# Kernel optimization log

Hardware: AMD Instinct MI355X
Metric: run time of the kernel (lower is better)

The kernel has to match this reference:

```python
import jax, jax.numpy as jnp
import numpy as np

N, E = 50000, 600000
IN_DIM, HID, OUT = 512, 256, 64
NEG_SLOPE = 0.2  # pyg GATConv default negative_slope


def setup_inputs() -> dict:
    key = jax.random.key(0)
    ks = jax.random.split(key, 6)
    features = jax.random.normal(ks[0], (N, IN_DIM), jnp.float32)
    edge_index = jax.random.randint(ks[1], (2, E), 0, N)
    W1 = jax.random.normal(ks[2], (IN_DIM, HID), jnp.float32) * (1.0 / np.sqrt(IN_DIM))
    W2 = jax.random.normal(ks[3], (HID, OUT), jnp.float32) * (1.0 / np.sqrt(HID))
    att_src = jax.random.normal(ks[4], (HID,), jnp.float32) * 0.1
    att_dst = jax.random.normal(ks[5], (HID,), jnp.float32) * 0.1
    return {"features": features, "W1": W1, "W2": W2,
            "att_src": att_src, "att_dst": att_dst, "edge_index": edge_index}


def _gat_propagate(h_pre, a_src, a_dst, src, dst, n):
    """STAGATE GATConv message passing (heads=1, concat=False, no self loops).

    Per-edge logit = leaky_relu(alpha_src[src] + alpha_dst[dst]),
    softmax over edges sharing the same dst, scatter-add of weighted src feats.
    """
    logits = jax.nn.leaky_relu(a_src[src] + a_dst[dst], NEG_SLOPE)        # [E]
    m = jax.ops.segment_max(logits, dst, num_segments=n)                   # [N]
    ex = jnp.exp(logits - m[dst])                                          # [E]
    denom = jax.ops.segment_sum(ex, dst, num_segments=n)                   # [N]
    w = ex / (denom[dst] + 1e-16)                                          # [E], pyg softmax eps
    return jax.ops.segment_sum(h_pre[src] * w[:, None], dst, num_segments=n)  # [N, C]


def reference(features, W1, W2, att_src, att_dst, edge_index):
    src, dst = edge_index[0], edge_index[1]
    n = features.shape[0]
    # conv1: attention computed and cached (self.attentions)
    hp1 = features @ W1                      # [N, HID]
    a_s = hp1 @ att_src                      # [N] per-node src attention score
    a_d = hp1 @ att_dst                      # [N] per-node dst attention score
    h1 = jax.nn.elu(_gat_propagate(hp1, a_s, a_d, src, dst, n))
    # conv2: attention=False -> plain linear
    h2 = h1 @ W2                             # [N, OUT]
    # conv3: weights = conv2.lin_src.T, tied_attention = conv1.attentions
    hp3 = h2 @ W2.T                          # [N, HID]
    h3 = jax.nn.elu(_gat_propagate(hp3, a_s, a_d, src, dst, n))
    # conv4: weights = conv1.lin_src.T, attention=False
    h4 = h3 @ W1.T                           # [N, IN_DIM]
    return (h2, h4)
```

## Files before the change

### kernel.cpp

```cpp
#include <hip/hip_runtime.h>
#include <hip/hip_bf16.h>
#include <cstdint>
#include <cstddef>

#define IN_DIM 512
#define HID 256
#define OUTD 64
#define NEG_SLOPE 0.2f

typedef __attribute__((ext_vector_type(8))) __bf16 bfrag_t;
typedef __attribute__((ext_vector_type(4))) float facc_t;
typedef __attribute__((ext_vector_type(4))) unsigned int u32x4;

__device__ __forceinline__ float bf2f(unsigned short u) {
  return __uint_as_float(((unsigned int)u) << 16);
}
__device__ __forceinline__ unsigned short f2bf(float f) {
  unsigned int x = __float_as_uint(f);
  x = (x + 0x7FFFu + ((x >> 16) & 1u)) >> 16;
  return (unsigned short)x;
}

#define GLOAD_LDS16(g, l)                                              \
  __builtin_amdgcn_global_load_lds(                                    \
      (const __attribute__((address_space(1))) void*)(g),              \
      (__attribute__((address_space(3))) void*)(l), 16, 0, 0)

template <int BM, int BN>
__global__ __launch_bounds__(256) void gemm_bt(const unsigned short* __restrict__ A,
                                               const unsigned short* __restrict__ B,
                                               void* __restrict__ Craw,
                                               unsigned short* __restrict__ Cb,
                                               int M, int N, int K, int c32, int act) {
  constexpr int FM = BM / 32, FN = BN / 32;
  constexpr int RT = BM + BN;
  __shared__ __align__(16) unsigned short lds[RT * 32];

  const int bm0 = blockIdx.x * BM;
  const int bn0 = blockIdx.y * BN;
  const int tid = threadIdx.x;
  const int lane = tid & 63;
  const int wave = tid >> 6;
  const int wrow = (wave >> 1) * (BM / 2);
  const int wcol = (wave & 1) * (BN / 2);
  const int lr = lane & 15;
  const int quad = lane >> 4;
  const int swz = (quad ^ (lr & 3)) << 3;

  facc_t acc[FM][FN];
#pragma unroll
  for (int i = 0; i < FM; ++i)
#pragma unroll
    for (int j = 0; j < FN; ++j) acc[i][j] = (facc_t){0.f, 0.f, 0.f, 0.f};

  for (int k0 = 0; k0 < K; k0 += 32) {
    __syncthreads();
#pragma unroll
    for (int t = wave; t < RT / 16; t += 4) {
      const int r0 = t * 16;
      const int row = r0 + (lane >> 2);
      const int seg = (lane & 3) ^ (row & 3);
      const unsigned short* g;
      if (r0 < BM) {
        int gm = bm0 + row;
        if (gm >= M) gm = M - 1;
        g = A + (size_t)gm * K + k0 + seg * 8;
      } else {
        g = B + (size_t)(bn0 + row - BM) * K + k0 + seg * 8;
      }
      GLOAD_LDS16(g, lds + t * 512);
    }
    __syncthreads();

    bfrag_t a[FM], b[FN];
#pragma unroll
    for (int i = 0; i < FM; ++i)
      a[i] = *(const bfrag_t*)&lds[(wrow + i * 16 + lr) * 32 + swz];
#pragma unroll
    for (int j = 0; j < FN; ++j)
      b[j] = *(const bfrag_t*)&lds[(BM + wcol + j * 16 + lr) * 32 + swz];
#pragma unroll
    for (int i = 0; i < FM; ++i)
#pragma unroll
      for (int j = 0; j < FN; ++j)
        acc[i][j] = __builtin_amdgcn_mfma_f32_16x16x32_bf16(a[i], b[j], acc[i][j], 0, 0, 0);
  }

#pragma unroll
  for (int i = 0; i < FM; ++i)
#pragma unroll
    for (int r = 0; r < 4; ++r) {
      const int grow = bm0 + wrow + i * 16 + quad * 4 + r;
      if (grow < M) {
#pragma unroll
        for (int j = 0; j < FN; ++j) {
          const int gcol = bn0 + wcol + j * 16 + lr;
          float v = acc[i][j][r];
          if (act) v = v > 0.f ? v : (expf(v) - 1.f);
          if (c32) ((float*)Craw)[(size_t)grow * N + gcol] = v;
          else ((unsigned short*)Craw)[(size_t)grow * N + gcol] = f2bf(v);
          if (Cb) Cb[(size_t)grow * N + gcol] = f2bf(v);
        }
      }
    }
}

__global__ void cvt_feat(const float* __restrict__ in, unsigned short* __restrict__ out,
                         int n8) {
  const int i = blockIdx.x * 256 + threadIdx.x;
  if (i >= n8) return;
  const float4 f0 = ((const float4*)in)[i * 2];
  const float4 f1 = ((const float4*)in)[i * 2 + 1];
  u32x4 pk;
  pk.x = (unsigned int)f2bf(f0.x) | ((unsigned int)f2bf(f0.y) << 16);
  pk.y = (unsigned int)f2bf(f0.z) | ((unsigned int)f2bf(f0.w) << 16);
  pk.z = (unsigned int)f2bf(f1.x) | ((unsigned int)f2bf(f1.y) << 16);
  pk.w = (unsigned int)f2bf(f1.z) | ((unsigned int)f2bf(f1.w) << 16);
  ((u32x4*)out)[i] = pk;
}

__global__ void cvt_weights(const float* __restrict__ W1, const float* __restrict__ W2,
                            unsigned short* __restrict__ W1T, unsigned short* __restrict__ W1b,
                            unsigned short* __restrict__ W2T, unsigned short* __restrict__ W2b) {
  const int idx = blockIdx.x * 256 + threadIdx.x;
  if (idx < IN_DIM * HID) {
    const unsigned short b = f2bf(W1[idx]);
    W1b[idx] = b;
    const int r = idx >> 8, c = idx & 255;
    W1T[(size_t)c * IN_DIM + r] = b;
  }
  if (idx < HID * OUTD) {
    const unsigned short b = f2bf(W2[idx]);
    W2b[idx] = b;
    const int r = idx >> 6, c = idx & 63;
    W2T[(size_t)c * HID + r] = b;
  }
}

__global__ __launch_bounds__(256) void rowdot(const unsigned short* __restrict__ hp,
                                              const float* __restrict__ att_s,
                                              const float* __restrict__ att_d,
                                              float* __restrict__ as_, float* __restrict__ ad_,
                                              int n) {
  const int node = blockIdx.x * 4 + (threadIdx.x >> 6);
  if (node >= n) return;
  const int lane = threadIdx.x & 63;
  const unsigned short* row = hp + (size_t)node * HID + (lane << 2);
  float s = 0.f, d = 0.f;
#pragma unroll
  for (int j = 0; j < 4; ++j) {
    const float h = bf2f(row[j]);
    s += h * att_s[(lane << 2) + j];
    d += h * att_d[(lane << 2) + j];
  }
  for (int off = 32; off > 0; off >>= 1) {
    s += __shfl_down(s, off);
    d += __shfl_down(d, off);
  }
  if (lane == 0) { as_[node] = s; ad_[node] = d; }
}

__global__ void init_nodes(float* __restrict__ denom, int* __restrict__ deg, int n) {
  const int i = blockIdx.x * 256 + threadIdx.x;
  if (i < n) {
    denom[i] = 0.f;
    deg[i] = 0;
  }
}

__global__ void edge_pass1(const int* __restrict__ src, const int* __restrict__ dst,
                           const float* __restrict__ as_, const float* __restrict__ ad_,
                           float* __restrict__ eexp, float* __restrict__ denom,
                           int* __restrict__ deg, int E, int n) {
  const int e = blockIdx.x * 256 + threadIdx.x;
  if (e >= E) return;
  const int s = src[e], d = dst[e];
  if ((unsigned)s >= (unsigned)n || (unsigned)d >= (unsigned)n) return;
  float l = as_[s] + ad_[d];
  l = l > 0.f ? l : NEG_SLOPE * l;
  const float ex = expf(fminf(l, 60.f));
  eexp[e] = ex;
  atomicAdd(&denom[d], ex);
  atomicAdd(&deg[d], 1);
}

__global__ __launch_bounds__(256) void scan_reduce(const int* __restrict__ deg,
                                                   int* __restrict__ bsum, int n) {
  __shared__ int ws4[4];
  const int tid = threadIdx.x, lane = tid & 63, wid = tid >> 6;
  const int base = blockIdx.x * 2048 + tid * 8;
  int s = 0;
#pragma unroll
  for (int j = 0; j < 8; ++j) {
    const int i = base + j;
    if (i < n) s += deg[i];
  }
  for (int off = 32; off > 0; off >>= 1) s += __shfl_down(s, off);
  if (lane == 0) ws4[wid] = s;
  __syncthreads();
  if (tid == 0) bsum[blockIdx.x] = ws4[0] + ws4[1] + ws4[2] + ws4[3];
}

__global__ __launch_bounds__(256) void scan_final(const int* __restrict__ deg,
                                                  const int* __restrict__ bsum,
                                                  int* __restrict__ row_ptr,
                                                  int* __restrict__ cursor, int n) {
  __shared__ int wsum[4];
  __shared__ int blockoff;
  const int tid = threadIdx.x, lane = tid & 63, wid = tid >> 6;
  if (wid == 0) {
    int v = (lane < blockIdx.x) ? bsum[lane] : 0;
    for (int off = 32; off > 0; off >>= 1) v += __shfl_down(v, off);
    if (lane == 0) blockoff = v;
  }
  const int base = blockIdx.x * 2048 + tid * 8;
  int v[8], s = 0;
#pragma unroll
  for (int j = 0; j < 8; ++j) {
    const int i = base + j;
    v[j] = (i < n) ? deg[i] : 0;
    s += v[j];
  }
  int ws = s;
  for (int off = 1; off < 64; off <<= 1) {
    const int t = __shfl_up(ws, off);
    if (lane >= off) ws += t;
  }
  if (lane == 63) wsum[wid] = ws;
  __syncthreads();
  int woff = 0;
  for (int w_ = 0; w_ < wid; ++w_) woff += wsum[w_];
  int run = blockoff + woff + (ws - s);
#pragma unroll
  for (int j = 0; j < 8; ++j) {
    const int i = base + j;
    if (i < n) {
      cursor[i] = run;
      row_ptr[i + 1] = run + v[j];
    }
    run += v[j];
  }
  if (blockIdx.x == 0 && tid == 0) row_ptr[0] = 0;
}

__global__ void edge_scatter(const int* __restrict__ src, const int* __restrict__ dst,
                             const float* __restrict__ eexp, const float* __restrict__ denom,
                             int* __restrict__ cursor, int* __restrict__ csr_src,
                             float* __restrict__ csr_w, int E, int n) {
  const int e = blockIdx.x * 256 + threadIdx.x;
  if (e >= E) return;
  const int s = src[e], d = dst[e];
  if ((unsigned)s >= (unsigned)n || (unsigned)d >= (unsigned)n) return;
  const float w = eexp[e] / (denom[d] + 1e-16f);
  const int pos = atomicAdd(&cursor[d], 1);
  csr_src[pos] = s;
  csr_w[pos] = w;
}

__global__ __launch_bounds__(256) void gat_prop256(const unsigned short* __restrict__ hpre,
                                                   const int* __restrict__ row_ptr,
                                                   const int* __restrict__ csr_src,
                                                   const float* __restrict__ csr_w,
                                                   unsigned short* __restrict__ out, int n) {
  const int node = blockIdx.x * 4 + (threadIdx.x >> 6);
  if (node >= n) return;
  const int lane = threadIdx.x & 63;
  const int half = lane >> 5;
  const int lh = lane & 31;
  const int beg = row_ptr[node], end = row_ptr[node + 1];
  const unsigned short* base = hpre + (lh << 3);
  float a[8] = {0.f, 0.f, 0.f, 0.f, 0.f, 0.f, 0.f, 0.f};
  int e = beg;
  for (; e + 8 <= end; e += 8) {
#pragma unroll
    for (int u = 0; u < 4; ++u) {
      const int e2 = e + 2 * u + half;
      const int s = csr_src[e2];
      const float w = csr_w[e2];
      const u32x4 v = *(const u32x4*)(base + (size_t)s * HID);
      a[0] += w * bf2f((unsigned short)(v.x & 0xffffu));
      a[1] += w * bf2f((unsigned short)(v.x >> 16));
      a[2] += w * bf2f((unsigned short)(v.y & 0xffffu));
      a[3] += w * bf2f((unsigned short)(v.y >> 16));
      a[4] += w * bf2f((unsigned short)(v.z & 0xffffu));
      a[5] += w * bf2f((unsigned short)(v.z >> 16));
      a[6] += w * bf2f((unsigned short)(v.w & 0xffffu));
      a[7] += w * bf2f((unsigned short)(v.w >> 16));
    }
  }
  for (; e < end; e += 2) {
    const int e2 = e + half;
    if (e2 < end) {
      const int s = csr_src[e2];
      const float w = csr_w[e2];
      const u32x4 v = *(const u32x4*)(base + (size_t)s * HID);
      a[0] += w * bf2f((unsigned short)(v.x & 0xffffu));
      a[1] += w * bf2f((unsigned short)(v.x >> 16));
      a[2] += w * bf2f((unsigned short)(v.y & 0xffffu));
      a[3] += w * bf2f((unsigned short)(v.y >> 16));
      a[4] += w * bf2f((unsigned short)(v.z & 0xffffu));
      a[5] += w * bf2f((unsigned short)(v.z >> 16));
      a[6] += w * bf2f((unsigned short)(v.w & 0xffffu));
      a[7] += w * bf2f((unsigned short)(v.w >> 16));
    }
  }
#pragma unroll
  for (int i = 0; i < 8; ++i) a[i] += __shfl_xor(a[i], 32);
  if (half == 0) {
#pragma unroll
    for (int i = 0; i < 8; ++i) a[i] = a[i] > 0.f ? a[i] : (expf(a[i]) - 1.f);
    u32x4 o;
    o.x = (unsigned int)f2bf(a[0]) | ((unsigned int)f2bf(a[1]) << 16);
    o.y = (unsigned int)f2bf(a[2]) | ((unsigned int)f2bf(a[3]) << 16);
    o.z = (unsigned int)f2bf(a[4]) | ((unsigned int)f2bf(a[5]) << 16);
    o.w = (unsigned int)f2bf(a[6]) | ((unsigned int)f2bf(a[7]) << 16);
    *(u32x4*)(out + (size_t)node * HID + (lh << 3)) = o;
  }
}

__global__ __launch_bounds__(256) void gat_prop64(const unsigned short* __restrict__ hpre,
                                                  const int* __restrict__ row_ptr,
                                                  const int* __restrict__ csr_src,
                                                  const float* __restrict__ csr_w,
                                                  unsigned short* __restrict__ out, int n) {
  const int node = blockIdx.x * 4 + (threadIdx.x >> 6);
  if (node >= n) return;
  const int lane = threadIdx.x & 63;
  const int quad = lane >> 4;
  const int lr = lane & 15;
  const int beg = row_ptr[node], end = row_ptr[node + 1];
  const unsigned short* base = hpre + (lr << 2);
  float a0 = 0.f, a1 = 0.f, a2 = 0.f, a3 = 0.f;
  int e = beg;
  for (; e + 8 <= end; e += 8) {
#pragma unroll
    for (int u = 0; u < 2; ++u) {
      const int e2 = e + 4 * u + quad;
      const int s = csr_src[e2];
      const float w = csr_w[e2];
      const uint2 v = *(const uint2*)(base + (size_t)s * OUTD);
      a0 += w * bf2f((unsigned short)(v.x & 0xffffu));
      a1 += w * bf2f((unsigned short)(v.x >> 16));
      a2 += w * bf2f((unsigned short)(v.y & 0xffffu));
      a3 += w * bf2f((unsigned short)(v.y >> 16));
    }
  }
  for (; e < end; e += 4) {
    const int e2 = e + quad;
    if (e2 < end) {
      const int s = csr_src[e2];
      const float w = csr_w[e2];
      const uint2 v = *(const uint2*)(base + (size_t)s * OUTD);
      a0 += w * bf2f((unsigned short)(v.x & 0xffffu));
      a1 += w * bf2f((unsigned short)(v.x >> 16));
      a2 += w * bf2f((unsigned short)(v.y & 0xffffu));
      a3 += w * bf2f((unsigned short)(v.y >> 16));
    }
  }
  a0 += __shfl_xor(a0, 16); a0 += __shfl_xor(a0, 32);
  a1 += __shfl_xor(a1, 16); a1 += __shfl_xor(a1, 32);
  a2 += __shfl_xor(a2, 16); a2 += __shfl_xor(a2, 32);
  a3 += __shfl_xor(a3, 16); a3 += __shfl_xor(a3, 32);
  if (quad == 0) {
    uint2 o;
    o.x = (unsigned int)f2bf(a0) | ((unsigned int)f2bf(a1) << 16);
    o.y = (unsigned int)f2bf(a2) | ((unsigned int)f2bf(a3) << 16);
    *(uint2*)(out + (size_t)node * OUTD + (lr << 2)) = o;
  }
}

extern "C" void kernel_launch(void* const* d_in, const int* in_sizes, int n_in,
                              void* d_out, int out_size, void* d_ws, size_t ws_size,
                              hipStream_t stream) {
  const float* feat = (const float*)d_in[0];
  const float* W1 = (const float*)d_in[1];
  const float* W2 = (const float*)d_in[2];
  const float* att_s = (const float*)d_in[3];
  const float* att_d = (const float*)d_in[4];
  const int* ei = (const int*)d_in[5];
  const int N = in_sizes[0] / IN_DIM;
  const int E = in_sizes[5] / 2;
  const int* src = ei;
  const int* dst = ei + E;
  float* outf = (float*)d_out;

  unsigned short* featb = (unsigned short*)(outf + (size_t)N * OUTD);
  unsigned short* hp1 = featb + (size_t)N * IN_DIM;
  unsigned short* g2 = hp1 + (size_t)N * HID;

  char* w = (char*)d_ws;
  size_t off = 0;
  auto alloc = [&](size_t bytes) -> void* {
    void* p = w + off;
    off += (bytes + 255) & ~(size_t)255;
    return p;
  };
  unsigned short* h1h3 = (unsigned short*)alloc((size_t)N * HID * 2);
  unsigned short* h2b = (unsigned short*)alloc((size_t)N * OUTD * 2);
  float* a_src_v = (float*)alloc((size_t)N * 4);
  float* a_dst_v = (float*)alloc((size_t)N * 4);
  float* eexp = (float*)alloc((size_t)E * 4);
  float* denom = (float*)alloc((size_t)N * 4);
  int* deg = (int*)alloc((size_t)N * 4);
  int* row_ptr = (int*)alloc((size_t)(N + 1) * 4);
  int* cursor = (int*)alloc((size_t)N * 4);
  int* bsum = (int*)alloc((size_t)64 * 4);
  int* csr_src = (int*)alloc((size_t)E * 4);
  float* csr_w = (float*)alloc((size_t)E * 4);
  unsigned short* W1T = (unsigned short*)alloc((size_t)IN_DIM * HID * 2);
  unsigned short* W1b = (unsigned short*)alloc((size_t)IN_DIM * HID * 2);
  unsigned short* W2T = (unsigned short*)alloc((size_t)HID * OUTD * 2);
  unsigned short* W2b = (unsigned short*)alloc((size_t)HID * OUTD * 2);

  const int EB = (E + 255) / 256;
  const int NB = (N + 255) / 256;
  const int MB = (N + 127) / 128;
  const int SB = (N + 2047) / 2048;

  cvt_feat<<<(N * IN_DIM / 8 + 255) / 256, 256, 0, stream>>>(feat, featb, N * IN_DIM / 8);
  cvt_weights<<<(IN_DIM * HID + 255) / 256, 256, 0, stream>>>(W1, W2, W1T, W1b, W2T, W2b);

  gemm_bt<128, 128><<<dim3(MB, HID / 128), 256, 0, stream>>>(featb, W1T, hp1, nullptr,
                                                             N, HID, IN_DIM, 0, 0);
  rowdot<<<(N + 3) / 4, 256, 0, stream>>>(hp1, att_s, att_d, a_src_v, a_dst_v, N);

  init_nodes<<<NB, 256, 0, stream>>>(denom, deg, N);
  edge_pass1<<<EB, 256, 0, stream>>>(src, dst, a_src_v, a_dst_v, eexp, denom, deg, E, N);
  scan_reduce<<<SB, 256, 0, stream>>>(deg, bsum, N);
  scan_final<<<SB, 256, 0, stream>>>(deg, bsum, row_ptr, cursor, N);
  edge_scatter<<<EB, 256, 0, stream>>>(src, dst, eexp, denom, cursor, csr_src, csr_w, E, N);

  gat_prop256<<<(N + 3) / 4, 256, 0, stream>>>(hp1, row_ptr, csr_src, csr_w, h1h3, N);
  gemm_bt<128, 64><<<dim3(MB, OUTD / 64), 256, 0, stream>>>(h1h3, W2T, outf, h2b,
                                                            N, OUTD, HID, 1, 0);
  gat_prop64<<<(N + 3) / 4, 256, 0, stream>>>(h2b, row_ptr, csr_src, csr_w, g2, N);
  gemm_bt<128, 128><<<dim3(MB, HID / 128), 256, 0, stream>>>(g2, W2b, h1h3, nullptr,
                                                             N, HID, OUTD, 0, 1);
  gemm_bt<128, 128><<<dim3(MB, IN_DIM / 128), 256, 0, stream>>>(h1h3, W1b,
                                                                outf + (size_t)N * OUTD,
                                                                nullptr, N, IN_DIM, HID, 1, 0);
}
```

Baseline: 502.8 us.

## Fuse feature bf16 conversion into first GEMM and defer softmax normalization

Drops the separate fp32-to-bf16 feature conversion pass. The first GEMM now reads fp32 features directly and converts them to bf16 while staging into LDS. The per-destination softmax denominator atomics are removed: normalization is computed inside the propagation kernels by summing the edge weights, which takes the separate denom init and the divide out of edge_scatter. Source index and weight are packed into one int2 CSR array so each edge needs a single load. The trade-off is that the first GEMM now does synchronous register loads for A instead of the async LDS path, and each propagation pass recomputes the weight sum.

```diff
diff --git a/kernel.cpp b/kernel.cpp
--- a/kernel.cpp
+++ b/kernel.cpp
@@ -105,18 +105,89 @@
     }
 }
 
-__global__ void cvt_feat(const float* __restrict__ in, unsigned short* __restrict__ out,
-                         int n8) {
-  const int i = blockIdx.x * 256 + threadIdx.x;
-  if (i >= n8) return;
-  const float4 f0 = ((const float4*)in)[i * 2];
-  const float4 f1 = ((const float4*)in)[i * 2 + 1];
-  u32x4 pk;
-  pk.x = (unsigned int)f2bf(f0.x) | ((unsigned int)f2bf(f0.y) << 16);
-  pk.y = (unsigned int)f2bf(f0.z) | ((unsigned int)f2bf(f0.w) << 16);
-  pk.z = (unsigned int)f2bf(f1.x) | ((unsigned int)f2bf(f1.y) << 16);
-  pk.w = (unsigned int)f2bf(f1.z) | ((unsigned int)f2bf(f1.w) << 16);
-  ((u32x4*)out)[i] = pk;
+template <int BM, int BN>
+__global__ __launch_bounds__(256) void gemm_a32_bt(const float* __restrict__ A,
+                                                   const unsigned short* __restrict__ B,
+                                                   unsigned short* __restrict__ C,
+                                                   int M, int N, int K) {
+  constexpr int FM = BM / 32, FN = BN / 32;
+  constexpr int RT = BM + BN;
+  __shared__ __align__(16) unsigned short lds[RT * 32];
+
+  const int bm0 = blockIdx.x * BM;
+  const int bn0 = blockIdx.y * BN;
+  const int tid = threadIdx.x;
+  const int lane = tid & 63;
+  const int wave = tid >> 6;
+  const int wrow = (wave >> 1) * (BM / 2);
+  const int wcol = (wave & 1) * (BN / 2);
+  const int lr = lane & 15;
+  const int quad = lane >> 4;
+  const int swz = (quad ^ (lr & 3)) << 3;
+
+  const int arow0 = tid >> 2;
+  const int aseg = tid & 3;
+
+  facc_t acc[FM][FN];
+#pragma unroll
+  for (int i = 0; i < FM; ++i)
+#pragma unroll
+    for (int j = 0; j < FN; ++j) acc[i][j] = (facc_t){0.f, 0.f, 0.f, 0.f};
+
+  for (int k0 = 0; k0 < K; k0 += 32) {
+    __syncthreads();
+#pragma unroll
+    for (int t = wave; t < BN / 16; t += 4) {
+      const int lr0 = BM + t * 16;
+      const int row = lr0 + (lane >> 2);
+      const int seg = (lane & 3) ^ (row & 3);
+      const unsigned short* g = B + (size_t)(bn0 + t * 16 + (lane >> 2)) * K + k0 + seg * 8;
+      GLOAD_LDS16(g, lds + lr0 * 32);
+    }
+#pragma unroll
+    for (int h = 0; h < 2; ++h) {
+      const int row = arow0 + h * (BM / 2);
+      int gm = bm0 + row;
+      if (gm >= M) gm = M - 1;
+      const float* g = A + (size_t)gm * K + k0 + aseg * 8;
+      const float4 fa = ((const float4*)g)[0];
+      const float4 fb = ((const float4*)g)[1];
+      u32x4 pk;
+      pk.x = (unsigned int)f2bf(fa.x) | ((unsigned int)f2bf(fa.y) << 16);
+      pk.y = (unsigned int)f2bf(fa.z) | ((unsigned int)f2bf(fa.w) << 16);
+      pk.z = (unsigned int)f2bf(fb.x) | ((unsigned int)f2bf(fb.y) << 16);
+      pk.w = (unsigned int)f2bf(fb.z) | ((unsigned int)f2bf(fb.w) << 16);
+      *(u32x4*)&lds[row * 32 + ((aseg ^ (row & 3)) << 3)] = pk;
+    }
+    __syncthreads();
+
+    bfrag_t a[FM], b[FN];
+#pragma unroll
+    for (int i = 0; i < FM; ++i)
+      a[i] = *(const bfrag_t*)&lds[(wrow + i * 16 + lr) * 32 + swz];
+#pragma unroll
+    for (int j = 0; j < FN; ++j)
+      b[j] = *(const bfrag_t*)&lds[(BM + wcol + j * 16 + lr) * 32 + swz];
+#pragma unroll
+    for (int i = 0; i < FM; ++i)
+#pragma unroll
+      for (int j = 0; j < FN; ++j)
+        acc[i][j] = __builtin_amdgcn_mfma_f32_16x16x32_bf16(a[i], b[j], acc[i][j], 0, 0, 0);
+  }
+
+#pragma unroll
+  for (int i = 0; i < FM; ++i)
+#pragma unroll
+    for (int r = 0; r < 4; ++r) {
+      const int grow = bm0 + wrow + i * 16 + quad * 4 + r;
+      if (grow < M) {
+#pragma unroll
+        for (int j = 0; j < FN; ++j) {
+          const int gcol = bn0 + wcol + j * 16 + lr;
+          C[(size_t)grow * N + gcol] = f2bf(acc[i][j][r]);
+        }
+      }
+    }
 }
 
 __global__ void cvt_weights(const float* __restrict__ W1, const float* __restrict__ W2,
@@ -160,27 +231,21 @@
   if (lane == 0) { as_[node] = s; ad_[node] = d; }
 }
 
-__global__ void init_nodes(float* __restrict__ denom, int* __restrict__ deg, int n) {
+__global__ void init_deg(int* __restrict__ deg, int n) {
   const int i = blockIdx.x * 256 + threadIdx.x;
-  if (i < n) {
-    denom[i] = 0.f;
-    deg[i] = 0;
-  }
+  if (i < n) deg[i] = 0;
 }
 
 __global__ void edge_pass1(const int* __restrict__ src, const int* __restrict__ dst,
                            const float* __restrict__ as_, const float* __restrict__ ad_,
-                           float* __restrict__ eexp, float* __restrict__ denom,
-                           int* __restrict__ deg, int E, int n) {
+                           float* __restrict__ eexp, int* __restrict__ deg, int E, int n) {
   const int e = blockIdx.x * 256 + threadIdx.x;
   if (e >= E) return;
   const int s = src[e], d = dst[e];
   if ((unsigned)s >= (unsigned)n || (unsigned)d >= (unsigned)n) return;
   float l = as_[s] + ad_[d];
   l = l > 0.f ? l : NEG_SLOPE * l;
-  const float ex = expf(fminf(l, 60.f));
-  eexp[e] = ex;
-  atomicAdd(&denom[d], ex);
+  eexp[e] = expf(fminf(l, 60.f));
   atomicAdd(&deg[d], 1);
 }
 
@@ -244,23 +309,22 @@
 }
 
 __global__ void edge_scatter(const int* __restrict__ src, const int* __restrict__ dst,
-                             const float* __restrict__ eexp, const float* __restrict__ denom,
-                             int* __restrict__ cursor, int* __restrict__ csr_src,
-                             float* __restrict__ csr_w, int E, int n) {
+                             const float* __restrict__ eexp, int* __restrict__ cursor,
+                             int2* __restrict__ csr, int E, int n) {
   const int e = blockIdx.x * 256 + threadIdx.x;
   if (e >= E) return;
   const int s = src[e], d = dst[e];
   if ((unsigned)s >= (unsigned)n || (unsigned)d >= (unsigned)n) return;
-  const float w = eexp[e] / (denom[d] + 1e-16f);
   const int pos = atomicAdd(&cursor[d], 1);
-  csr_src[pos] = s;
-  csr_w[pos] = w;
+  int2 c;
+  c.x = s;
+  c.y = __float_as_int(eexp[e]);
+  csr[pos] = c;
 }
 
 __global__ __launch_bounds__(256) void gat_prop256(const unsigned short* __restrict__ hpre,
                                                    const int* __restrict__ row_ptr,
-                                                   const int* __restrict__ csr_src,
-                                                   const float* __restrict__ csr_w,
+                                                   const int2* __restrict__ csr,
                                                    unsigned short* __restrict__ out, int n) {
   const int node = blockIdx.x * 4 + (threadIdx.x >> 6);
   if (node >= n) return;
@@ -270,14 +334,15 @@
   const int beg = row_ptr[node], end = row_ptr[node + 1];
   const unsigned short* base = hpre + (lh << 3);
   float a[8] = {0.f, 0.f, 0.f, 0.f, 0.f, 0.f, 0.f, 0.f};
+  float wsum = 0.f;
   int e = beg;
   for (; e + 8 <= end; e += 8) {
 #pragma unroll
     for (int u = 0; u < 4; ++u) {
-      const int e2 = e + 2 * u + half;
-      const int s = csr_src[e2];
-      const float w = csr_w[e2];
-      const u32x4 v = *(const u32x4*)(base + (size_t)s * HID);
+      const int2 c = csr[e + 2 * u + half];
+      const float w = __int_as_float(c.y);
+      const u32x4 v = *(const u32x4*)(base + (size_t)c.x * HID);
+      wsum += w;
       a[0] += w * bf2f((unsigned short)(v.x & 0xffffu));
       a[1] += w * bf2f((unsigned short)(v.x >> 16));
       a[2] += w * bf2f((unsigned short)(v.y & 0xffffu));
@@ -291,9 +356,10 @@
   for (; e < end; e += 2) {
     const int e2 = e + half;
     if (e2 < end) {
-      const int s = csr_src[e2];
-      const float w = csr_w[e2];
-      const u32x4 v = *(const u32x4*)(base + (size_t)s * HID);
+      const int2 c = csr[e2];
+      const float w = __int_as_float(c.y);
+      const u32x4 v = *(const u32x4*)(base + (size_t)c.x * HID);
+      wsum += w;
       a[0] += w * bf2f((unsigned short)(v.x & 0xffffu));
       a[1] += w * bf2f((unsigned short)(v.x >> 16));
       a[2] += w * bf2f((unsigned short)(v.y & 0xffffu));
@@ -306,9 +372,14 @@
   }
 #pragma unroll
   for (int i = 0; i < 8; ++i) a[i] += __shfl_xor(a[i], 32);
+  wsum += __shfl_xor(wsum, 32);
   if (half == 0) {
-#pragma unroll
-    for (int i = 0; i < 8; ++i) a[i] = a[i] > 0.f ? a[i] : (expf(a[i]) - 1.f);
+    const float inv = 1.f / (wsum + 1e-16f);
+#pragma unroll
+    for (int i = 0; i < 8; ++i) {
+      a[i] *= inv;
+      a[i] = a[i] > 0.f ? a[i] : (expf(a[i]) - 1.f);
+    }
     u32x4 o;
     o.x = (unsigned int)f2bf(a[0]) | ((unsigned int)f2bf(a[1]) << 16);
     o.y = (unsigned int)f2bf(a[2]) | ((unsigned int)f2bf(a[3]) << 16);
@@ -320,8 +391,7 @@
 
 __global__ __launch_bounds__(256) void gat_prop64(const unsigned short* __restrict__ hpre,
                                                   const int* __restrict__ row_ptr,
-                                                  const int* __restrict__ csr_src,
-                                                  const float* __restrict__ csr_w,
+                                                  const int2* __restrict__ csr,
                                                   unsigned short* __restrict__ out, int n) {
   const int node = blockIdx.x * 4 + (threadIdx.x >> 6);
   if (node >= n) return;
@@ -330,15 +400,15 @@
   const int lr = lane & 15;
   const int beg = row_ptr[node], end = row_ptr[node + 1];
   const unsigned short* base = hpre + (lr << 2);
-  float a0 = 0.f, a1 = 0.f, a2 = 0.f, a3 = 0.f;
+  float a0 = 0.f, a1 = 0.f, a2 = 0.f, a3 = 0.f, wsum = 0.f;
   int e = beg;
   for (; e + 8 <= end; e += 8) {
 #pragma unroll
     for (int u = 0; u < 2; ++u) {
-      const int e2 = e + 4 * u + quad;
-      const int s = csr_src[e2];
-      const float w = csr_w[e2];
-      const uint2 v = *(const uint2*)(base + (size_t)s * OUTD);
+      const int2 c = csr[e + 4 * u + quad];
+      const float w = __int_as_float(c.y);
+      const uint2 v = *(const uint2*)(base + (size_t)c.x * OUTD);
+      wsum += w;
       a0 += w * bf2f((unsigned short)(v.x & 0xffffu));
       a1 += w * bf2f((unsigned short)(v.x >> 16));
       a2 += w * bf2f((unsigned short)(v.y & 0xffffu));
@@ -348,9 +418,10 @@
   for (; e < end; e += 4) {
     const int e2 = e + quad;
     if (e2 < end) {
-      const int s = csr_src[e2];
-      const float w = csr_w[e2];
-      const uint2 v = *(const uint2*)(base + (size_t)s * OUTD);
+      const int2 c = csr[e2];
+      const float w = __int_as_float(c.y);
+      const uint2 v = *(const uint2*)(base + (size_t)c.x * OUTD);
+      wsum += w;
       a0 += w * bf2f((unsigned short)(v.x & 0xffffu));
       a1 += w * bf2f((unsigned short)(v.x >> 16));
       a2 += w * bf2f((unsigned short)(v.y & 0xffffu));
@@ -361,10 +432,12 @@
   a1 += __shfl_xor(a1, 16); a1 += __shfl_xor(a1, 32);
   a2 += __shfl_xor(a2, 16); a2 += __shfl_xor(a2, 32);
   a3 += __shfl_xor(a3, 16); a3 += __shfl_xor(a3, 32);
+  wsum += __shfl_xor(wsum, 16); wsum += __shfl_xor(wsum, 32);
   if (quad == 0) {
+    const float inv = 1.f / (wsum + 1e-16f);
     uint2 o;
-    o.x = (unsigned int)f2bf(a0) | ((unsigned int)f2bf(a1) << 16);
-    o.y = (unsigned int)f2bf(a2) | ((unsigned int)f2bf(a3) << 16);
+    o.x = (unsigned int)f2bf(a0 * inv) | ((unsigned int)f2bf(a1 * inv) << 16);
+    o.y = (unsigned int)f2bf(a2 * inv) | ((unsigned int)f2bf(a3 * inv) << 16);
     *(uint2*)(out + (size_t)node * OUTD + (lr << 2)) = o;
   }
 }
@@ -384,8 +457,7 @@
   const int* dst = ei + E;
   float* outf = (float*)d_out;
 
-  unsigned short* featb = (unsigned short*)(outf + (size_t)N * OUTD);
-  unsigned short* hp1 = featb + (size_t)N * IN_DIM;
+  unsigned short* hp1 = (unsigned short*)(outf + (size_t)N * OUTD);
   unsigned short* g2 = hp1 + (size_t)N * HID;
 
   char* w = (char*)d_ws;
@@ -400,13 +472,11 @@
   float* a_src_v = (float*)alloc((size_t)N * 4);
   float* a_dst_v = (float*)alloc((size_t)N * 4);
   float* eexp = (float*)alloc((size_t)E * 4);
-  float* denom = (float*)alloc((size_t)N * 4);
   int* deg = (int*)alloc((size_t)N * 4);
   int* row_ptr = (int*)alloc((size_t)(N + 1) * 4);
   int* cursor = (int*)alloc((size_t)N * 4);
   int* bsum = (int*)alloc((size_t)64 * 4);
-  int* csr_src = (int*)alloc((size_t)E * 4);
-  float* csr_w = (float*)alloc((size_t)E * 4);
+  int2* csr = (int2*)alloc((size_t)E * 8);
   unsigned short* W1T = (unsigned short*)alloc((size_t)IN_DIM * HID * 2);
   unsigned short* W1b = (unsigned short*)alloc((size_t)IN_DIM * HID * 2);
   unsigned short* W2T = (unsigned short*)alloc((size_t)HID * OUTD * 2);
@@ -417,23 +487,22 @@
   const int MB = (N + 127) / 128;
   const int SB = (N + 2047) / 2048;
 
-  cvt_feat<<<(N * IN_DIM / 8 + 255) / 256, 256, 0, stream>>>(feat, featb, N * IN_DIM / 8);
   cvt_weights<<<(IN_DIM * HID + 255) / 256, 256, 0, stream>>>(W1, W2, W1T, W1b, W2T, W2b);
 
-  gemm_bt<128, 128><<<dim3(MB, HID / 128), 256, 0, stream>>>(featb, W1T, hp1, nullptr,
-                                                             N, HID, IN_DIM, 0, 0);
+  gemm_a32_bt<128, 128><<<dim3(MB, HID / 128), 256, 0, stream>>>(feat, W1T, hp1,
+                                                                 N, HID, IN_DIM);
   rowdot<<<(N + 3) / 4, 256, 0, stream>>>(hp1, att_s, att_d, a_src_v, a_dst_v, N);
 
-  init_nodes<<<NB, 256, 0, stream>>>(denom, deg, N);
-  edge_pass1<<<EB, 256, 0, stream>>>(src, dst, a_src_v, a_dst_v, eexp, denom, deg, E, N);
+  init_deg<<<NB, 256, 0, stream>>>(deg, N);
+  edge_pass1<<<EB, 256, 0, stream>>>(src, dst, a_src_v, a_dst_v, eexp, deg, E, N);
   scan_reduce<<<SB, 256, 0, stream>>>(deg, bsum, N);
   scan_final<<<SB, 256, 0, stream>>>(deg, bsum, row_ptr, cursor, N);
-  edge_scatter<<<EB, 256, 0, stream>>>(src, dst, eexp, denom, cursor, csr_src, csr_w, E, N);
-
-  gat_prop256<<<(N + 3) / 4, 256, 0, stream>>>(hp1, row_ptr, csr_src, csr_w, h1h3, N);
+  edge_scatter<<<EB, 256, 0, stream>>>(src, dst, eexp, cursor, csr, E, N);
+
+  gat_prop256<<<(N + 3) / 4, 256, 0, stream>>>(hp1, row_ptr, csr, h1h3, N);
   gemm_bt<128, 64><<<dim3(MB, OUTD / 64), 256, 0, stream>>>(h1h3, W2T, outf, h2b,
                                                             N, OUTD, HID, 1, 0);
-  gat_prop64<<<(N + 3) / 4, 256, 0, stream>>>(h2b, row_ptr, csr_src, csr_w, g2, N);
+  gat_prop64<<<(N + 3) / 4, 256, 0, stream>>>(h2b, row_ptr, csr, g2, N);
   gemm_bt<128, 128><<<dim3(MB, HID / 128), 256, 0, stream>>>(g2, W2b, h1h3, nullptr,
                                                              N, HID, OUTD, 0, 1);
   gemm_bt<128, 128><<<dim3(MB, IN_DIM / 128), 256, 0, stream>>>(h1h3, W1b,
```

New measurement: 451.4 us. 10.2% less time.
